# Optimization experiments

Hardware: AMD Instinct MI355X
Metric: run time of the kernel (lower is better)

Reference implementation:

```python
import jax, jax.numpy as jnp
import numpy as np

N_NODES = 100000
N_EDGES = 1600000
D_IN = 128
UNITS = 128


def setup_inputs() -> dict:
    key = jax.random.key(0)
    k1, k2, k3, k4, k5 = jax.random.split(key, 5)
    x = jax.random.normal(k1, (N_NODES, D_IN), dtype=jnp.float32)
    # glorot-uniform-like dense weight
    limit = float(np.sqrt(6.0 / (D_IN + UNITS)))
    w = jax.random.uniform(k2, (D_IN, UNITS), minval=-limit, maxval=limit, dtype=jnp.float32)
    # COO sparse adjacency: A[row, col] = val
    edge_row = jax.random.randint(k3, (N_EDGES,), 0, N_NODES, dtype=jnp.int32)
    edge_col = jax.random.randint(k4, (N_EDGES,), 0, N_NODES, dtype=jnp.int32)
    edge_val = jax.random.uniform(k5, (N_EDGES,), dtype=jnp.float32)
    return {"x": x, "w": w, "edge_row": edge_row, "edge_col": edge_col, "edge_val": edge_val}


def reference(x, w, edge_row, edge_col, edge_val):
    # dropout rate = 0.0 -> identity (module default)
    xw = x @ w                                   # [N, units] dense projection
    # sparse adjacency propagation: out[i] = sum_e val[e] * xw[col[e]] for row[e]==i
    msgs = xw[edge_col] * edge_val[:, None]      # [E, units] irregular gather
    out = jax.ops.segment_sum(msgs, edge_row, num_segments=x.shape[0])
    return jax.nn.relu(out)                      # activation
```

## Files before the change

kernel.cpp:

```cpp
#include <hip/hip_runtime.h>

#define N_NODES 100000
#define N_EDGES 1600000
#define D 128
#define NB 512
#define BCAP 3584
#define BSTRIDE 16
#define CHUNK 4000
#define NSCAT 400
#define NGEMM 1563
#define HCAP 1792

typedef __attribute__((ext_vector_type(8))) short  short8;
typedef __attribute__((ext_vector_type(4))) float  floatx4;

__device__ __forceinline__ ushort f2bf(float f) {
    unsigned u = __float_as_uint(f);
    u += 0x7FFF + ((u >> 16) & 1);
    return (ushort)(u >> 16);
}
__device__ __forceinline__ float bf2f(ushort s) {
    return __uint_as_float((unsigned)s << 16);
}
__device__ __forceinline__ int bucket_of(int r)  { return (int)(((unsigned)r << 9) / 100000u); }
__device__ __forceinline__ int row_start(int b)  { return (b * 100000 + 511) >> 9; }

union SMem {
    struct {
        int2  stage[CHUNK];
        int   sA[NB];
        int   sB[NB];
        int   lcur[NB];
        int   gbase[NB];
        short sbuck[CHUNK];
    } sc;
    ushort wt[128 * 128];
};

__global__ __launch_bounds__(256) void gemm_and_scatter(const float* __restrict__ x,
                                                        const float* __restrict__ w,
                                                        ushort* __restrict__ xwb,
                                                        const int* __restrict__ erow,
                                                        const int* __restrict__ ecol,
                                                        const float* __restrict__ eval,
                                                        int* __restrict__ bcnt,
                                                        int2* __restrict__ bkt) {
    __shared__ SMem sm;
    const int t = threadIdx.x;

    if (blockIdx.x < NGEMM) {
        ushort* wt = sm.wt;
        const int wv   = t >> 6;
        const int lane = t & 63;
        const int m    = lane & 15;
        const int q    = lane >> 4;

        {
            const float4* w4 = (const float4*)w;
            for (int i = t; i < 4096; i += 256) {
                const float4 v = w4[i];
                const int k = i >> 5;
                const int n = (i & 31) << 2;
                const int c = k >> 3, kc = k & 7;
#pragma unroll
                for (int d = 0; d < 4; ++d) {
                    const float val = (d == 0) ? v.x : (d == 1) ? v.y : (d == 2) ? v.z : v.w;
                    const int nn = n + d;
                    wt[(nn << 7) | (((c ^ (nn & 15)) & 15) << 3) | kc] = f2bf(val);
                }
            }
        }
        __syncthreads();

        const int rbase = blockIdx.x * 64 + wv * 16;
        if (rbase >= N_NODES) return;

        const float* xrow = x + (size_t)(rbase + m) * D;

        floatx4 acc[8];
#pragma unroll
        for (int tt = 0; tt < 8; ++tt) acc[tt] = (floatx4){0.f, 0.f, 0.f, 0.f};

#pragma unroll
        for (int kk = 0; kk < D; kk += 32) {
            const float4 a0 = *(const float4*)(xrow + kk + q * 8);
            const float4 a1 = *(const float4*)(xrow + kk + q * 8 + 4);
            short8 a;
            a[0] = (short)f2bf(a0.x); a[1] = (short)f2bf(a0.y);
            a[2] = (short)f2bf(a0.z); a[3] = (short)f2bf(a0.w);
            a[4] = (short)f2bf(a1.x); a[5] = (short)f2bf(a1.y);
            a[6] = (short)f2bf(a1.z); a[7] = (short)f2bf(a1.w);

#pragma unroll
            for (int tt = 0; tt < 8; ++tt) {
                const int n  = tt * 16 + m;
                const int cc = (((kk >> 3) + q) ^ m) & 15;
                const short8 b = *(const short8*)&wt[(n << 7) | (cc << 3)];
                acc[tt] = __builtin_amdgcn_mfma_f32_16x16x32_bf16(a, b, acc[tt], 0, 0, 0);
            }
        }

#pragma unroll
        for (int tt = 0; tt < 8; ++tt) {
#pragma unroll
            for (int r = 0; r < 4; ++r) {
                xwb[(size_t)(rbase + q * 4 + r) * D + tt * 16 + m] = f2bf(acc[tt][r]);
            }
        }
    } else {
        const int e0 = (blockIdx.x - NGEMM) * CHUNK;
        int*   sA    = sm.sc.sA;
        int*   sB    = sm.sc.sB;
        int*   lcur  = sm.sc.lcur;
        int*   gbase = sm.sc.gbase;
        short* sbuck = sm.sc.sbuck;
        int2*  stage = sm.sc.stage;

        sA[t] = 0; sA[t + 256] = 0;
        __syncthreads();

        for (int i = t; i < CHUNK; i += 256) {
            atomicAdd(&sA[bucket_of(erow[e0 + i])], 1);
        }
        __syncthreads();

        int cur = 0;
        int* bufs[2] = {sA, sB};
#pragma unroll
        for (int o = 1; o < 512; o <<= 1) {
            const int* src = bufs[cur];
            int*       dst = bufs[cur ^ 1];
            const int i0 = t, i1 = t + 256;
            dst[i0] = src[i0] + ((i0 >= o) ? src[i0 - o] : 0);
            dst[i1] = src[i1] + ((i1 >= o) ? src[i1 - o] : 0);
            cur ^= 1;
            __syncthreads();
        }
        {
            const int* incl = bufs[cur];
            int*       excl = bufs[cur ^ 1];
            excl[t]       = (t == 0) ? 0 : incl[t - 1];
            excl[t + 256] = incl[t + 255];
        }
        __syncthreads();
        int* L = bufs[cur ^ 1];

        for (int b = t; b < NB; b += 256) {
            lcur[b] = L[b];
            const int cnt = ((b == NB - 1) ? CHUNK : L[b + 1]) - L[b];
            gbase[b] = (cnt > 0) ? atomicAdd(&bcnt[b * BSTRIDE], cnt) : 0;
        }
        __syncthreads();

        for (int i = t; i < CHUNK; i += 256) {
            const int   r = erow[e0 + i];
            const int   c = ecol[e0 + i];
            const float v = eval[e0 + i];
            const int   b = bucket_of(r);
            const int  rl = r - row_start(b);
            const int pos = atomicAdd(&lcur[b], 1);
            stage[pos] = make_int2((rl << 17) | c, __float_as_int(v));
            sbuck[pos] = (short)b;
        }
        __syncthreads();

        for (int i = t; i < CHUNK; i += 256) {
            const int b   = sbuck[i];
            const int dst = gbase[b] + (i - L[b]);
            if (dst < BCAP) bkt[(size_t)b * BCAP + dst] = stage[i];
        }
    }
}

__global__ __launch_bounds__(256, 4) void csr_gather(const int* __restrict__ bcnt,
                                                     const int2* __restrict__ bkt,
                                                     const ushort* __restrict__ xwb,
                                                     float* __restrict__ out) {
    __shared__ int2 lcsr[HCAP];
    __shared__ int  sA[256], sB[256], lcur[256];
    const int bg = blockIdx.x;
    const int b  = bg >> 1;
    const int h  = bg & 1;
    const int t  = threadIdx.x;
    const int n  = min(bcnt[b * BSTRIDE], BCAP);
    const int r0    = row_start(b);
    const int nrows = row_start(b + 1) - r0;
    const int mid   = (nrows + 1) >> 1;
    const int lo    = h ? mid : 0;
    const int hi    = h ? nrows : mid;
    const int nloc  = hi - lo;

    const int2* src = bkt + (size_t)b * BCAP;
    sA[t] = 0;
    __syncthreads();

    for (int i = t; i < n; i += 256) {
        const int rl = (int)(((unsigned)src[i].x) >> 17);
        if (rl >= lo && rl < hi) atomicAdd(&sA[rl - lo], 1);
    }
    __syncthreads();

    int cur = 0;
    int* bufs[2] = {sA, sB};
#pragma unroll
    for (int o = 1; o < 256; o <<= 1) {
        const int* s = bufs[cur];
        int*       d = bufs[cur ^ 1];
        d[t] = s[t] + ((t >= o) ? s[t - o] : 0);
        cur ^= 1;
        __syncthreads();
    }
    lcur[t] = (t == 0) ? 0 : bufs[cur][t - 1];
    __syncthreads();

    for (int i = t; i < n; i += 256) {
        const int2 e = src[i];
        const int rl = (int)(((unsigned)e.x) >> 17);
        if (rl >= lo && rl < hi) {
            const int pos = atomicAdd(&lcur[rl - lo], 1);
            if (pos < HCAP) lcsr[pos] = make_int2(e.x & 0x1FFFF, e.y);
        }
    }
    __syncthreads();

    const int qid = t >> 4;
    const int lc  = (t & 15) << 3;

    for (int ln = qid; ln < nloc; ln += 16) {
        int start = (ln == 0) ? 0 : lcur[ln - 1];
        int end   = lcur[ln];
        start = min(start, HCAP);
        end   = min(end, HCAP);

        float acc[8] = {0, 0, 0, 0, 0, 0, 0, 0};

        for (int j = start; j < end; j += 4) {
            const int jb = j + 1, jc = j + 2, jd = j + 3;
            const int2 e0 = lcsr[j];
            const int2 e1 = lcsr[min(jb, end - 1)];
            const int2 e2 = lcsr[min(jc, end - 1)];
            const int2 e3 = lcsr[min(jd, end - 1)];
            const short8 m0 = *(const short8*)&xwb[(size_t)e0.x * D + lc];
            const short8 m1 = *(const short8*)&xwb[(size_t)e1.x * D + lc];
            const short8 m2 = *(const short8*)&xwb[(size_t)e2.x * D + lc];
            const short8 m3 = *(const short8*)&xwb[(size_t)e3.x * D + lc];
            const float v0 = __int_as_float(e0.y);
            const float v1 = (jb < end) ? __int_as_float(e1.y) : 0.f;
            const float v2 = (jc < end) ? __int_as_float(e2.y) : 0.f;
            const float v3 = (jd < end) ? __int_as_float(e3.y) : 0.f;
#pragma unroll
            for (int i = 0; i < 8; ++i) {
                acc[i] += v0 * bf2f((ushort)m0[i]);
                acc[i] += v1 * bf2f((ushort)m1[i]);
                acc[i] += v2 * bf2f((ushort)m2[i]);
                acc[i] += v3 * bf2f((ushort)m3[i]);
            }
        }

        float* o = out + (size_t)(r0 + lo + ln) * D + lc;
        *(float4*)(o + 0) = make_float4(fmaxf(acc[0], 0.f), fmaxf(acc[1], 0.f),
                                        fmaxf(acc[2], 0.f), fmaxf(acc[3], 0.f));
        *(float4*)(o + 4) = make_float4(fmaxf(acc[4], 0.f), fmaxf(acc[5], 0.f),
                                        fmaxf(acc[6], 0.f), fmaxf(acc[7], 0.f));
    }
}

extern "C" void kernel_launch(void* const* d_in, const int* in_sizes, int n_in,
                              void* d_out, int out_size, void* d_ws, size_t ws_size,
                              hipStream_t stream) {
    const float* x    = (const float*)d_in[0];
    const float* w    = (const float*)d_in[1];
    const int*   erow = (const int*)d_in[2];
    const int*   ecol = (const int*)d_in[3];
    const float* eval = (const float*)d_in[4];
    float*       out  = (float*)d_out;

    char*   ws_base = (char*)d_ws;
    ushort* xwb  = (ushort*)ws_base;
    int*    bcnt = (int*)(ws_base + 25600000);
    int2*   bkt  = (int2*)(ws_base + 25632768);

    (void)hipMemsetAsync(bcnt, 0, 32768, stream);

    gemm_and_scatter<<<NGEMM + NSCAT, 256, 0, stream>>>(x, w, xwb, erow, ecol, eval, bcnt, bkt);
    csr_gather<<<NB * 2, 256, 0, stream>>>(bcnt, bkt, xwb, out);
}
```

Baseline: 225.4 us.

## Replace bucket sort with per-row fixed-capacity edge slots via global atomics

The two-level bucketed COO-to-CSR conversion is removed: its shared-memory histogram, prefix scans and staging in the scatter blocks, and the per-bucket local re-sort in the gather kernel. Each edge now claims a slot in a fixed 44-entry per-row array through a global atomic on a per-row counter. The gather kernel becomes one 16-thread group per row, with no shared memory and a higher occupancy hint. This trades the scan and sync overhead for 1.6M random global atomics and uncoalesced 8-byte writes. Rows with more than 44 edges would silently drop edges.

```diff
diff --git a/kernel.cpp b/kernel.cpp
--- a/kernel.cpp
+++ b/kernel.cpp
@@ -3,13 +3,11 @@
 #define N_NODES 100000
 #define N_EDGES 1600000
 #define D 128
-#define NB 512
-#define BCAP 3584
-#define BSTRIDE 16
 #define CHUNK 4000
 #define NSCAT 400
 #define NGEMM 1563
-#define HCAP 1792
+#define CAP 44
+#define RSTRIDE 2
 
 typedef __attribute__((ext_vector_type(8))) short  short8;
 typedef __attribute__((ext_vector_type(4))) float  floatx4;
@@ -22,20 +20,6 @@
 __device__ __forceinline__ float bf2f(ushort s) {
     return __uint_as_float((unsigned)s << 16);
 }
-__device__ __forceinline__ int bucket_of(int r)  { return (int)(((unsigned)r << 9) / 100000u); }
-__device__ __forceinline__ int row_start(int b)  { return (b * 100000 + 511) >> 9; }
-
-union SMem {
-    struct {
-        int2  stage[CHUNK];
-        int   sA[NB];
-        int   sB[NB];
-        int   lcur[NB];
-        int   gbase[NB];
-        short sbuck[CHUNK];
-    } sc;
-    ushort wt[128 * 128];
-};
 
 __global__ __launch_bounds__(256) void gemm_and_scatter(const float* __restrict__ x,
                                                         const float* __restrict__ w,
@@ -43,13 +27,12 @@
                                                         const int* __restrict__ erow,
                                                         const int* __restrict__ ecol,
                                                         const float* __restrict__ eval,
-                                                        int* __restrict__ bcnt,
+                                                        int* __restrict__ rcnt,
                                                         int2* __restrict__ bkt) {
-    __shared__ SMem sm;
+    __shared__ ushort wt[128 * 128];
     const int t = threadIdx.x;
 
     if (blockIdx.x < NGEMM) {
-        ushort* wt = sm.wt;
         const int wv   = t >> 6;
         const int lane = t & 63;
         const int m    = lane & 15;
@@ -109,160 +92,63 @@
         }
     } else {
         const int e0 = (blockIdx.x - NGEMM) * CHUNK;
-        int*   sA    = sm.sc.sA;
-        int*   sB    = sm.sc.sB;
-        int*   lcur  = sm.sc.lcur;
-        int*   gbase = sm.sc.gbase;
-        short* sbuck = sm.sc.sbuck;
-        int2*  stage = sm.sc.stage;
-
-        sA[t] = 0; sA[t + 256] = 0;
-        __syncthreads();
-
-        for (int i = t; i < CHUNK; i += 256) {
-            atomicAdd(&sA[bucket_of(erow[e0 + i])], 1);
-        }
-        __syncthreads();
-
-        int cur = 0;
-        int* bufs[2] = {sA, sB};
-#pragma unroll
-        for (int o = 1; o < 512; o <<= 1) {
-            const int* src = bufs[cur];
-            int*       dst = bufs[cur ^ 1];
-            const int i0 = t, i1 = t + 256;
-            dst[i0] = src[i0] + ((i0 >= o) ? src[i0 - o] : 0);
-            dst[i1] = src[i1] + ((i1 >= o) ? src[i1 - o] : 0);
-            cur ^= 1;
-            __syncthreads();
-        }
-        {
-            const int* incl = bufs[cur];
-            int*       excl = bufs[cur ^ 1];
-            excl[t]       = (t == 0) ? 0 : incl[t - 1];
-            excl[t + 256] = incl[t + 255];
-        }
-        __syncthreads();
-        int* L = bufs[cur ^ 1];
-
-        for (int b = t; b < NB; b += 256) {
-            lcur[b] = L[b];
-            const int cnt = ((b == NB - 1) ? CHUNK : L[b + 1]) - L[b];
-            gbase[b] = (cnt > 0) ? atomicAdd(&bcnt[b * BSTRIDE], cnt) : 0;
-        }
-        __syncthreads();
-
-        for (int i = t; i < CHUNK; i += 256) {
-            const int   r = erow[e0 + i];
-            const int   c = ecol[e0 + i];
-            const float v = eval[e0 + i];
-            const int   b = bucket_of(r);
-            const int  rl = r - row_start(b);
-            const int pos = atomicAdd(&lcur[b], 1);
-            stage[pos] = make_int2((rl << 17) | c, __float_as_int(v));
-            sbuck[pos] = (short)b;
-        }
-        __syncthreads();
-
-        for (int i = t; i < CHUNK; i += 256) {
-            const int b   = sbuck[i];
-            const int dst = gbase[b] + (i - L[b]);
-            if (dst < BCAP) bkt[(size_t)b * BCAP + dst] = stage[i];
+        for (int i = t; i < CHUNK / 2; i += 256) {
+            const int ia = e0 + i;
+            const int ib = ia + CHUNK / 2;
+            const int   ra = erow[ia];
+            const int   rb = erow[ib];
+            const int   ca = ecol[ia];
+            const int   cb = ecol[ib];
+            const float va = eval[ia];
+            const float vb = eval[ib];
+            const int sa = atomicAdd(&rcnt[ra * RSTRIDE], 1);
+            const int sb = atomicAdd(&rcnt[rb * RSTRIDE], 1);
+            if (sa < CAP) bkt[(size_t)ra * CAP + sa] = make_int2(ca, __float_as_int(va));
+            if (sb < CAP) bkt[(size_t)rb * CAP + sb] = make_int2(cb, __float_as_int(vb));
         }
     }
 }
 
-__global__ __launch_bounds__(256, 4) void csr_gather(const int* __restrict__ bcnt,
+__global__ __launch_bounds__(256, 8) void row_gather(const int* __restrict__ rcnt,
                                                      const int2* __restrict__ bkt,
                                                      const ushort* __restrict__ xwb,
                                                      float* __restrict__ out) {
-    __shared__ int2 lcsr[HCAP];
-    __shared__ int  sA[256], sB[256], lcur[256];
-    const int bg = blockIdx.x;
-    const int b  = bg >> 1;
-    const int h  = bg & 1;
-    const int t  = threadIdx.x;
-    const int n  = min(bcnt[b * BSTRIDE], BCAP);
-    const int r0    = row_start(b);
-    const int nrows = row_start(b + 1) - r0;
-    const int mid   = (nrows + 1) >> 1;
-    const int lo    = h ? mid : 0;
-    const int hi    = h ? nrows : mid;
-    const int nloc  = hi - lo;
+    const int t   = threadIdx.x;
+    const int r   = blockIdx.x * 16 + (t >> 4);
+    const int lc  = (t & 15) << 3;
+    const int deg = min(rcnt[r * RSTRIDE], CAP);
+    const int2* eb = bkt + (size_t)r * CAP;
 
-    const int2* src = bkt + (size_t)b * BCAP;
-    sA[t] = 0;
-    __syncthreads();
+    float acc[8] = {0, 0, 0, 0, 0, 0, 0, 0};
 
-    for (int i = t; i < n; i += 256) {
-        const int rl = (int)(((unsigned)src[i].x) >> 17);
-        if (rl >= lo && rl < hi) atomicAdd(&sA[rl - lo], 1);
-    }
-    __syncthreads();
-
-    int cur = 0;
-    int* bufs[2] = {sA, sB};
+    for (int j = 0; j < deg; j += 4) {
+        const int jb = j + 1, jc = j + 2, jd = j + 3;
+        const int2 e0 = eb[j];
+        const int2 e1 = eb[min(jb, deg - 1)];
+        const int2 e2 = eb[min(jc, deg - 1)];
+        const int2 e3 = eb[min(jd, deg - 1)];
+        const short8 m0 = *(const short8*)&xwb[(size_t)e0.x * D + lc];
+        const short8 m1 = *(const short8*)&xwb[(size_t)e1.x * D + lc];
+        const short8 m2 = *(const short8*)&xwb[(size_t)e2.x * D + lc];
+        const short8 m3 = *(const short8*)&xwb[(size_t)e3.x * D + lc];
+        const float v0 = __int_as_float(e0.y);
+        const float v1 = (jb < deg) ? __int_as_float(e1.y) : 0.f;
+        const float v2 = (jc < deg) ? __int_as_float(e2.y) : 0.f;
+        const float v3 = (jd < deg) ? __int_as_float(e3.y) : 0.f;
 #pragma unroll
-    for (int o = 1; o < 256; o <<= 1) {
-        const int* s = bufs[cur];
-        int*       d = bufs[cur ^ 1];
-        d[t] = s[t] + ((t >= o) ? s[t - o] : 0);
-        cur ^= 1;
-        __syncthreads();
-    }
-    lcur[t] = (t == 0) ? 0 : bufs[cur][t - 1];
-    __syncthreads();
-
-    for (int i = t; i < n; i += 256) {
-        const int2 e = src[i];
-        const int rl = (int)(((unsigned)e.x) >> 17);
-        if (rl >= lo && rl < hi) {
-            const int pos = atomicAdd(&lcur[rl - lo], 1);
-            if (pos < HCAP) lcsr[pos] = make_int2(e.x & 0x1FFFF, e.y);
+        for (int i = 0; i < 8; ++i) {
+            acc[i] += v0 * bf2f((ushort)m0[i]);
+            acc[i] += v1 * bf2f((ushort)m1[i]);
+            acc[i] += v2 * bf2f((ushort)m2[i]);
+            acc[i] += v3 * bf2f((ushort)m3[i]);
         }
     }
-    __syncthreads();
 
-    const int qid = t >> 4;
-    const int lc  = (t & 15) << 3;
-
-    for (int ln = qid; ln < nloc; ln += 16) {
-        int start = (ln == 0) ? 0 : lcur[ln - 1];
-        int end   = lcur[ln];
-        start = min(start, HCAP);
-        end   = min(end, HCAP);
-
-        float acc[8] = {0, 0, 0, 0, 0, 0, 0, 0};
-
-        for (int j = start; j < end; j += 4) {
-            const int jb = j + 1, jc = j + 2, jd = j + 3;
-            const int2 e0 = lcsr[j];
-            const int2 e1 = lcsr[min(jb, end - 1)];
-            const int2 e2 = lcsr[min(jc, end - 1)];
-            const int2 e3 = lcsr[min(jd, end - 1)];
-            const short8 m0 = *(const short8*)&xwb[(size_t)e0.x * D + lc];
-            const short8 m1 = *(const short8*)&xwb[(size_t)e1.x * D + lc];
-            const short8 m2 = *(const short8*)&xwb[(size_t)e2.x * D + lc];
-            const short8 m3 = *(const short8*)&xwb[(size_t)e3.x * D + lc];
-            const float v0 = __int_as_float(e0.y);
-            const float v1 = (jb < end) ? __int_as_float(e1.y) : 0.f;
-            const float v2 = (jc < end) ? __int_as_float(e2.y) : 0.f;
-            const float v3 = (jd < end) ? __int_as_float(e3.y) : 0.f;
-#pragma unroll
-            for (int i = 0; i < 8; ++i) {
-                acc[i] += v0 * bf2f((ushort)m0[i]);
-                acc[i] += v1 * bf2f((ushort)m1[i]);
-                acc[i] += v2 * bf2f((ushort)m2[i]);
-                acc[i] += v3 * bf2f((ushort)m3[i]);
-            }
-        }
-
-        float* o = out + (size_t)(r0 + lo + ln) * D + lc;
-        *(float4*)(o + 0) = make_float4(fmaxf(acc[0], 0.f), fmaxf(acc[1], 0.f),
-                                        fmaxf(acc[2], 0.f), fmaxf(acc[3], 0.f));
-        *(float4*)(o + 4) = make_float4(fmaxf(acc[4], 0.f), fmaxf(acc[5], 0.f),
-                                        fmaxf(acc[6], 0.f), fmaxf(acc[7], 0.f));
-    }
+    float* o = out + (size_t)r * D + lc;
+    *(float4*)(o + 0) = make_float4(fmaxf(acc[0], 0.f), fmaxf(acc[1], 0.f),
+                                    fmaxf(acc[2], 0.f), fmaxf(acc[3], 0.f));
+    *(float4*)(o + 4) = make_float4(fmaxf(acc[4], 0.f), fmaxf(acc[5], 0.f),
+                                    fmaxf(acc[6], 0.f), fmaxf(acc[7], 0.f));
 }
 
 extern "C" void kernel_launch(void* const* d_in, const int* in_sizes, int n_in,
@@ -277,11 +163,11 @@
 
     char*   ws_base = (char*)d_ws;
     ushort* xwb  = (ushort*)ws_base;
-    int*    bcnt = (int*)(ws_base + 25600000);
-    int2*   bkt  = (int2*)(ws_base + 25632768);
+    int*    rcnt = (int*)(ws_base + 25600000);
+    int2*   bkt  = (int2*)(ws_base + 26400000);
 
-    (void)hipMemsetAsync(bcnt, 0, 32768, stream);
+    (void)hipMemsetAsync(rcnt, 0, 800000, stream);
 
-    gemm_and_scatter<<<NGEMM + NSCAT, 256, 0, stream>>>(x, w, xwb, erow, ecol, eval, bcnt, bkt);
-    csr_gather<<<NB * 2, 256, 0, stream>>>(bcnt, bkt, xwb, out);
+    gemm_and_scatter<<<NGEMM + NSCAT, 256, 0, stream>>>(x, w, xwb, erow, ecol, eval, rcnt, bkt);
+    row_gather<<<N_NODES / 16, 256, 0, stream>>>(rcnt, bkt, xwb, out);
 }
```

Result: slower. 272.0 us (+20.7%).

## Split fused GEMM/scatter kernel and stage GEMM output through LDS for coalesced stores

Applied to the files above, without the earlier changes.

Separates the combined GEMM and edge-bucketing kernel into two kernels launched back to back on the same stream. Each GEMM block now processes two 64-row tiles, so the weight-to-LDS conversion cost is amortised over twice as many rows. Output is staged through a per-wave LDS tile so each lane writes 16-byte vectors instead of scattered 2-byte stores. The trade-off is that the GEMM and scatter work no longer overlap within one launch, and the extra launch adds a serialization point.

```diff
diff --git a/kernel.cpp b/kernel.cpp
--- a/kernel.cpp
+++ b/kernel.cpp
@@ -8,7 +8,7 @@
 #define BSTRIDE 16
 #define CHUNK 4000
 #define NSCAT 400
-#define NGEMM 1563
+#define NGEMM 782
 #define HCAP 1792
 
 typedef __attribute__((ext_vector_type(8))) short  short8;
@@ -25,57 +25,40 @@
 __device__ __forceinline__ int bucket_of(int r)  { return (int)(((unsigned)r << 9) / 100000u); }
 __device__ __forceinline__ int row_start(int b)  { return (b * 100000 + 511) >> 9; }
 
-union SMem {
-    struct {
-        int2  stage[CHUNK];
-        int   sA[NB];
-        int   sB[NB];
-        int   lcur[NB];
-        int   gbase[NB];
-        short sbuck[CHUNK];
-    } sc;
-    ushort wt[128 * 128];
-};
-
-__global__ __launch_bounds__(256) void gemm_and_scatter(const float* __restrict__ x,
-                                                        const float* __restrict__ w,
-                                                        ushort* __restrict__ xwb,
-                                                        const int* __restrict__ erow,
-                                                        const int* __restrict__ ecol,
-                                                        const float* __restrict__ eval,
-                                                        int* __restrict__ bcnt,
-                                                        int2* __restrict__ bkt) {
-    __shared__ SMem sm;
-    const int t = threadIdx.x;
-
-    if (blockIdx.x < NGEMM) {
-        ushort* wt = sm.wt;
-        const int wv   = t >> 6;
-        const int lane = t & 63;
-        const int m    = lane & 15;
-        const int q    = lane >> 4;
-
-        {
-            const float4* w4 = (const float4*)w;
-            for (int i = t; i < 4096; i += 256) {
-                const float4 v = w4[i];
-                const int k = i >> 5;
-                const int n = (i & 31) << 2;
-                const int c = k >> 3, kc = k & 7;
-#pragma unroll
-                for (int d = 0; d < 4; ++d) {
-                    const float val = (d == 0) ? v.x : (d == 1) ? v.y : (d == 2) ? v.z : v.w;
-                    const int nn = n + d;
-                    wt[(nn << 7) | (((c ^ (nn & 15)) & 15) << 3) | kc] = f2bf(val);
-                }
-            }
-        }
-        __syncthreads();
-
-        const int rbase = blockIdx.x * 64 + wv * 16;
-        if (rbase >= N_NODES) return;
-
-        const float* xrow = x + (size_t)(rbase + m) * D;
+__global__ __launch_bounds__(256) void gemm_xw(const float* __restrict__ x,
+                                               const float* __restrict__ w,
+                                               ushort* __restrict__ xwb) {
+    __shared__ ushort wt[128 * 128];
+    __shared__ ushort ct[4][16 * 128];
+    const int t    = threadIdx.x;
+    const int wv   = t >> 6;
+    const int lane = t & 63;
+    const int m    = lane & 15;
+    const int q    = lane >> 4;
+
+    {
+        const float4* w4 = (const float4*)w;
+        for (int i = t; i < 4096; i += 256) {
+            const float4 v = w4[i];
+            const int k = i >> 5;
+            const int n = (i & 31) << 2;
+            const int c = k >> 3, kc = k & 7;
+#pragma unroll
+            for (int d = 0; d < 4; ++d) {
+                const float val = (d == 0) ? v.x : (d == 1) ? v.y : (d == 2) ? v.z : v.w;
+                const int nn = n + d;
+                wt[(nn << 7) | (((c ^ (nn & 15)) & 15) << 3) | kc] = f2bf(val);
+            }
+        }
+    }
+    __syncthreads();
+
+#pragma unroll
+    for (int tile = 0; tile < 2; ++tile) {
+        const int rbase = blockIdx.x * 128 + tile * 64 + wv * 16;
+        if (rbase >= N_NODES) break;
+
+        const float* xrow = x + (size_t)min(rbase + m, N_NODES - 1) * D;
 
         floatx4 acc[8];
 #pragma unroll
@@ -104,71 +87,86 @@
         for (int tt = 0; tt < 8; ++tt) {
 #pragma unroll
             for (int r = 0; r < 4; ++r) {
-                xwb[(size_t)(rbase + q * 4 + r) * D + tt * 16 + m] = f2bf(acc[tt][r]);
-            }
-        }
-    } else {
-        const int e0 = (blockIdx.x - NGEMM) * CHUNK;
-        int*   sA    = sm.sc.sA;
-        int*   sB    = sm.sc.sB;
-        int*   lcur  = sm.sc.lcur;
-        int*   gbase = sm.sc.gbase;
-        short* sbuck = sm.sc.sbuck;
-        int2*  stage = sm.sc.stage;
-
-        sA[t] = 0; sA[t + 256] = 0;
+                ct[wv][((q << 2) | r) * 128 + tt * 16 + m] = f2bf(acc[tt][r]);
+            }
+        }
+        const int rl  = lane >> 2;
+        const int ch  = lane & 3;
+        const int row = rbase + rl;
+        if (row < N_NODES) {
+            const ushort* srcp = &ct[wv][rl * 128 + ch * 32];
+            ushort*       dstp = &xwb[(size_t)row * D + ch * 32];
+#pragma unroll
+            for (int u = 0; u < 4; ++u) {
+                ((int4*)dstp)[u] = ((const int4*)srcp)[u];
+            }
+        }
+    }
+}
+
+__global__ __launch_bounds__(256) void bucket_scatter(const int* __restrict__ erow,
+                                                      const int* __restrict__ ecol,
+                                                      const float* __restrict__ eval,
+                                                      int* __restrict__ bcnt,
+                                                      int2* __restrict__ bkt) {
+    __shared__ int2  stage[CHUNK];
+    __shared__ int   sA[NB], sB[NB], lcur[NB], gbase[NB];
+    __shared__ short sbuck[CHUNK];
+    const int t  = threadIdx.x;
+    const int e0 = blockIdx.x * CHUNK;
+
+    sA[t] = 0; sA[t + 256] = 0;
+    __syncthreads();
+
+    for (int i = t; i < CHUNK; i += 256) {
+        atomicAdd(&sA[bucket_of(erow[e0 + i])], 1);
+    }
+    __syncthreads();
+
+    int cur = 0;
+    int* bufs[2] = {sA, sB};
+#pragma unroll
+    for (int o = 1; o < 512; o <<= 1) {
+        const int* src = bufs[cur];
+        int*       dst = bufs[cur ^ 1];
+        const int i0 = t, i1 = t + 256;
+        dst[i0] = src[i0] + ((i0 >= o) ? src[i0 - o] : 0);
+        dst[i1] = src[i1] + ((i1 >= o) ? src[i1 - o] : 0);
+        cur ^= 1;
         __syncthreads();
-
-        for (int i = t; i < CHUNK; i += 256) {
-            atomicAdd(&sA[bucket_of(erow[e0 + i])], 1);
-        }
-        __syncthreads();
-
-        int cur = 0;
-        int* bufs[2] = {sA, sB};
-#pragma unroll
-        for (int o = 1; o < 512; o <<= 1) {
-            const int* src = bufs[cur];
-            int*       dst = bufs[cur ^ 1];
-            const int i0 = t, i1 = t + 256;
-            dst[i0] = src[i0] + ((i0 >= o) ? src[i0 - o] : 0);
-            dst[i1] = src[i1] + ((i1 >= o) ? src[i1 - o] : 0);
-            cur ^= 1;
-            __syncthreads();
-        }
-        {
-            const int* incl = bufs[cur];
-            int*       excl = bufs[cur ^ 1];
-            excl[t]       = (t == 0) ? 0 : incl[t - 1];
-            excl[t + 256] = incl[t + 255];
-        }
-        __syncthreads();
-        int* L = bufs[cur ^ 1];
-
-        for (int b = t; b < NB; b += 256) {
-            lcur[b] = L[b];
-            const int cnt = ((b == NB - 1) ? CHUNK : L[b + 1]) - L[b];
-            gbase[b] = (cnt > 0) ? atomicAdd(&bcnt[b * BSTRIDE], cnt) : 0;
-        }
-        __syncthreads();
-
-        for (int i = t; i < CHUNK; i += 256) {
-            const int   r = erow[e0 + i];
-            const int   c = ecol[e0 + i];
-            const float v = eval[e0 + i];
-            const int   b = bucket_of(r);
-            const int  rl = r - row_start(b);
-            const int pos = atomicAdd(&lcur[b], 1);
-            stage[pos] = make_int2((rl << 17) | c, __float_as_int(v));
-            sbuck[pos] = (short)b;
-        }
-        __syncthreads();
-
-        for (int i = t; i < CHUNK; i += 256) {
-            const int b   = sbuck[i];
-            const int dst = gbase[b] + (i - L[b]);
-            if (dst < BCAP) bkt[(size_t)b * BCAP + dst] = stage[i];
-        }
+    }
+    {
+        const int* incl = bufs[cur];
+        int*       excl = bufs[cur ^ 1];
+        excl[t]       = (t == 0) ? 0 : incl[t - 1];
+        excl[t + 256] = incl[t + 255];
+    }
+    __syncthreads();
+    int* L = bufs[cur ^ 1];
+
+    for (int b = t; b < NB; b += 256) {
+        lcur[b] = L[b];
+        const int cnt = ((b == NB - 1) ? CHUNK : L[b + 1]) - L[b];
+        gbase[b] = (cnt > 0) ? atomicAdd(&bcnt[b * BSTRIDE], cnt) : 0;
+    }
+    __syncthreads();
+
+    for (int i = t; i < CHUNK; i += 256) {
+        const int   r = erow[e0 + i];
+        const int   c = ecol[e0 + i];
+        const float v = eval[e0 + i];
+        const int   b = bucket_of(r);
+        const int  rl = r - row_start(b);
+        const int pos = atomicAdd(&lcur[b], 1);
+        stage[pos] = make_int2((rl << 17) | c, __float_as_int(v));
+        sbuck[pos] = (short)b;
+    }
+    __syncthreads();
+
+    for (int i = t; i < CHUNK; i += 256) {
+        const int b   = sbuck[i];
+        const int dst = gbase[b] + (i - L[b]);
+        if (dst < BCAP) bkt[(size_t)b * BCAP + dst] = stage[i];
     }
 }
 
@@ -282,6 +280,7 @@
 
     (void)hipMemsetAsync(bcnt, 0, 32768, stream);
 
-    gemm_and_scatter<<<NGEMM + NSCAT, 256, 0, stream>>>(x, w, xwb, erow, ecol, eval, bcnt, bkt);
+    gemm_xw<<<NGEMM, 256, 0, stream>>>(x, w, xwb);
+    bucket_scatter<<<NSCAT, 256, 0, stream>>>(erow, ecol, eval, bcnt, bkt);
     csr_gather<<<NB * 2, 256, 0, stream>>>(bcnt, bkt, xwb, out);
 }
```

Result: slower. 232.0 us (+3.0%).

## Use persistent GEMM blocks and stage output through LDS for coalesced stores

Applied to the files above, without the earlier changes.

The GEMM part now runs in 512 persistent blocks that loop over the 64-row tiles. Each block loads and converts W into LDS once, instead of once per tile across 1563 blocks. Output tiles are written to a per-wave LDS buffer and then stored to global memory as 16-byte row chunks, replacing scattered 2-byte stores. This trades parallelism in the GEMM part for less W reload work and better-coalesced writes, and the larger LDS footprint may reduce occupancy.

```diff
diff --git a/kernel.cpp b/kernel.cpp
--- a/kernel.cpp
+++ b/kernel.cpp
@@ -8,7 +8,8 @@
 #define BSTRIDE 16
 #define CHUNK 4000
 #define NSCAT 400
-#define NGEMM 1563
+#define NGEMMB 512
+#define NTILES 1563
 #define HCAP 1792
 
 typedef __attribute__((ext_vector_type(8))) short  short8;
@@ -34,7 +35,10 @@
         int   gbase[NB];
         short sbuck[CHUNK];
     } sc;
-    ushort wt[128 * 128];
+    struct {
+        ushort wt[128 * 128];
+        ushort ct[4][16 * 128];
+    } ge;
 };
 
 __global__ __launch_bounds__(256) void gemm_and_scatter(const float* __restrict__ x,
@@ -48,8 +52,8 @@
     __shared__ SMem sm;
     const int t = threadIdx.x;
 
-    if (blockIdx.x < NGEMM) {
-        ushort* wt = sm.wt;
+    if (blockIdx.x < NGEMMB) {
+        ushort* wt = sm.ge.wt;
         const int wv   = t >> 6;
         const int lane = t & 63;
         const int m    = lane & 15;
@@ -72,43 +76,56 @@
         }
         __syncthreads();
 
-        const int rbase = blockIdx.x * 64 + wv * 16;
-        if (rbase >= N_NODES) return;
-
-        const float* xrow = x + (size_t)(rbase + m) * D;
-
-        floatx4 acc[8];
-#pragma unroll
-        for (int tt = 0; tt < 8; ++tt) acc[tt] = (floatx4){0.f, 0.f, 0.f, 0.f};
-
-#pragma unroll
-        for (int kk = 0; kk < D; kk += 32) {
-            const float4 a0 = *(const float4*)(xrow + kk + q * 8);
-            const float4 a1 = *(const float4*)(xrow + kk + q * 8 + 4);
-            short8 a;
-            a[0] = (short)f2bf(a0.x); a[1] = (short)f2bf(a0.y);
-            a[2] = (short)f2bf(a0.z); a[3] = (short)f2bf(a0.w);
-            a[4] = (short)f2bf(a1.x); a[5] = (short)f2bf(a1.y);
-            a[6] = (short)f2bf(a1.z); a[7] = (short)f2bf(a1.w);
+        for (int tb = blockIdx.x; tb < NTILES; tb += NGEMMB) {
+            const int rbase = tb * 64 + wv * 16;
+            if (rbase >= N_NODES) break;
+
+            const float* xrow = x + (size_t)min(rbase + m, N_NODES - 1) * D;
+
+            floatx4 acc[8];
+#pragma unroll
+            for (int tt = 0; tt < 8; ++tt) acc[tt] = (floatx4){0.f, 0.f, 0.f, 0.f};
+
+#pragma unroll
+            for (int kk = 0; kk < D; kk += 32) {
+                const float4 a0 = *(const float4*)(xrow + kk + q * 8);
+                const float4 a1 = *(const float4*)(xrow + kk + q * 8 + 4);
+                short8 a;
+                a[0] = (short)f2bf(a0.x); a[1] = (short)f2bf(a0.y);
+                a[2] = (short)f2bf(a0.z); a[3] = (short)f2bf(a0.w);
+                a[4] = (short)f2bf(a1.x); a[5] = (short)f2bf(a1.y);
+                a[6] = (short)f2bf(a1.z); a[7] = (short)f2bf(a1.w);
+
+#pragma unroll
+                for (int tt = 0; tt < 8; ++tt) {
+                    const int n  = tt * 16 + m;
+                    const int cc = (((kk >> 3) + q) ^ m) & 15;
+                    const short8 b = *(const short8*)&wt[(n << 7) | (cc << 3)];
+                    acc[tt] = __builtin_amdgcn_mfma_f32_16x16x32_bf16(a, b, acc[tt], 0, 0, 0);
+                }
+            }
 
 #pragma unroll
             for (int tt = 0; tt < 8; ++tt) {
-                const int n  = tt * 16 + m;
-                const int cc = (((kk >> 3) + q) ^ m) & 15;
-                const short8 b = *(const short8*)&wt[(n << 7) | (cc << 3)];
-                acc[tt] = __builtin_amdgcn_mfma_f32_16x16x32_bf16(a, b, acc[tt], 0, 0, 0);
-            }
-        }
-
-#pragma unroll
-        for (int tt = 0; tt < 8; ++tt) {
-#pragma unroll
-            for (int r = 0; r < 4; ++r) {
-                xwb[(size_t)(rbase + q * 4 + r) * D + tt * 16 + m] = f2bf(acc[tt][r]);
+#pragma unroll
+                for (int r = 0; r < 4; ++r) {
+                    sm.ge.ct[wv][((q << 2) | r) * 128 + tt * 16 + m] = f2bf(acc[tt][r]);
+                }
+            }
+            const int rl  = lane >> 2;
+            const int ch  = lane & 3;
+            const int row = rbase + rl;
+            if (row < N_NODES) {
+                const ushort* srcp = &sm.ge.ct[wv][rl * 128 + ch * 32];
+                ushort*       dstp = &xwb[(size_t)row * D + ch * 32];
+#pragma unroll
+                for (int u = 0; u < 4; ++u) {
+                    ((int4*)dstp)[u] = ((const int4*)srcp)[u];
+                }
             }
         }
     } else {
-        const int e0 = (blockIdx.x - NGEMM) * CHUNK;
+        const int e0 = (blockIdx.x - NGEMMB) * CHUNK;
         int*   sA    = sm.sc.sA;
         int*   sB    = sm.sc.sB;
         int*   lcur  = sm.sc.lcur;
@@ -282,6 +299,6 @@
 
     (void)hipMemsetAsync(bcnt, 0, 32768, stream);
 
-    gemm_and_scatter<<<NGEMM + NSCAT, 256, 0, stream>>>(x, w, xwb, erow, ecol, eval, bcnt, bkt);
+    gemm_and_scatter<<<NGEMMB + NSCAT, 256, 0, stream>>>(x, w, xwb, erow, ecol, eval, bcnt, bkt);
     csr_gather<<<NB * 2, 256, 0, stream>>>(bcnt, bkt, xwb, out);
 }
```

Measured after the change: 217.5 us. 1.04x faster.
